# Performance work log

Measured on AMD Instinct MI355X. Metric: run time of the kernel, lower is better.

## Reference

```python
import jax, jax.numpy as jnp
import numpy as np

S = 7          # grid size
B = 2          # boxes per cell
C = 20         # classes
STEP = 1.0 / S
L_COORD = 5.0
L_NOOBJ = 0.5
EPS = 1e-6


def setup_inputs() -> dict:
    key = jax.random.key(0)
    k1, k2, k3 = jax.random.split(key, 3)
    N = 16384
    pred = jax.random.normal(k1, (N, S, S, B * 5 + C), dtype=jnp.float32)
    target = jax.random.uniform(k2, (N, S, S, B * 5 + C), dtype=jnp.float32)
    objm = jax.random.uniform(k3, (N, S, S, B)) < 0.05
    tb = target[..., :10].reshape(N, S, S, B, 5)
    tb = tb.at[..., 4].set(tb[..., 4] * objm)
    target = target.at[..., :10].set(tb.reshape(N, S, S, 10))
    return {"pred": pred, "target": target}


def _convert_box(box, gx, gy):
    # box: [N,S,S,B,4] in cell-relative (x,y) + image-relative (w,h)
    # gx: grid x index (axis 2), gy: grid y index (axis 1); matches conver_box
    x = (box[..., 0] + gx) * STEP - box[..., 2] * 0.5
    y = (box[..., 1] + gy) * STEP - box[..., 3] * 0.5
    out = jnp.stack([x, y, box[..., 2], box[..., 3]], axis=-1)
    return jnp.clip(out, 0.0, 1.0)


def _iou(b1, b2):
    x1, y1, w1, h1 = b1[..., 0], b1[..., 1], b1[..., 2], b1[..., 3]
    x2, y2, w2, h2 = b2[..., 0], b2[..., 1], b2[..., 2], b2[..., 3]
    inter_w = jnp.maximum(w1 + w2 - (jnp.maximum(x1 + w1, x2 + w2) - jnp.minimum(x1, x2)), 0.0)
    inter_h = jnp.maximum(h1 + h2 - (jnp.maximum(y1 + h1, y2 + h2) - jnp.minimum(y1, y2)), 0.0)
    inter = inter_w * inter_h
    union = w1 * h1 + w2 * h2 - inter + EPS
    return inter / union


def reference(pred, target):
    N = pred.shape[0]
    pb = pred[..., :10].reshape(N, S, S, B, 5)   # [N,S,S,B,5]
    tb = target[..., :10].reshape(N, S, S, B, 5)
    pc = pred[..., 10:]                           # [N,S,S,C]
    tc = target[..., 10:]
    obj0 = tb[..., 4] > 0                         # [N,S,S,B]
    sig = jnp.any(obj0, axis=-1)                  # [N,S,S]
    # grid indices: torch loop uses (y=dim1, x=dim2), conver_box index=[x, y]
    gx = jnp.arange(S, dtype=pred.dtype).reshape(1, 1, S, 1)
    gy = jnp.arange(S, dtype=pred.dtype).reshape(1, S, 1, 1)
    ious = _iou(_convert_box(pb[..., :4], gx, gy), _convert_box(tb[..., :4], gx, gy))  # [N,S,S,B]
    # responsible box = argmax IoU (first index on ties, matching torch .max(0))
    best = jnp.argmax(ious, axis=-1)[..., None] == jnp.arange(B)  # [N,S,S,B]
    obj = obj0 & best
    zero = jnp.zeros((), pred.dtype)
    # confidence losses
    dconf2 = (pb[..., 4] - tb[..., 4]) ** 2
    obj_loss = jnp.sum(jnp.where(obj, dconf2, zero))
    noobj_loss = jnp.sum(jnp.where(~obj, dconf2, zero))
    # coordinate losses
    obj_e = obj[..., None]
    dxy2 = (pb[..., :2] - tb[..., :2]) ** 2
    xy_loss = jnp.sum(jnp.where(obj_e, dxy2, zero))
    pwh = jnp.maximum(pb[..., 2:4], 0.0)
    dwh2 = (jnp.sqrt(tb[..., 2:4] + EPS) - jnp.sqrt(pwh + EPS)) ** 2
    wh_loss = jnp.sum(jnp.where(obj_e, dwh2, zero))
    # class loss over cells containing any object
    dcls2 = (pc - tc) ** 2
    class_loss = jnp.sum(jnp.where(sig[..., None], dcls2, zero))
    loss = obj_loss + L_NOOBJ * noobj_loss + L_COORD * xy_loss + L_COORD * wh_loss + class_loss
    return loss / N
```

## Files before the change

kernel.cpp:

```cpp
#include <hip/hip_runtime.h>

#define STEPV (1.0f / 7.0f)
#define L_COORD 5.0f
#define L_NOOBJ 0.5f
#define EPSV 1e-6f

#define TILE 128
#define FLOATS_PER_CELL 30
#define TILE_FLOATS (TILE * FLOATS_PER_CELL)
#define TILE_F4 (TILE_FLOATS / 4)

__global__ __launch_bounds__(256) void yolo_loss_kernel(
    const float* __restrict__ pred,
    const float* __restrict__ tgt,
    float* __restrict__ partials)
{
    __shared__ float bufP[TILE_FLOATS];
    __shared__ float bufT[TILE_FLOATS];

    const int tid = threadIdx.x;
    const int base_f4 = blockIdx.x * TILE_F4;

    {
        const float4* srcP = reinterpret_cast<const float4*>(pred) + base_f4;
        const float4* srcT = reinterpret_cast<const float4*>(tgt) + base_f4;
        float4* dstP = reinterpret_cast<float4*>(bufP);
        float4* dstT = reinterpret_cast<float4*>(bufT);
        #pragma unroll
        for (int i = 0; i < (TILE_F4 + 255) / 256; ++i) {
            int li = tid + i * 256;
            if (li < TILE_F4) {
                dstP[li] = srcP[li];
                dstT[li] = srcT[li];
            }
        }
    }
    __syncthreads();

    const int cid  = tid & (TILE - 1);
    const int half = tid >> 7;
    const int cell = blockIdx.x * TILE + cid;

    float loss = 0.0f;

    if (half == 0) {
        const float* p = bufP + cid * FLOATS_PER_CELL;
        const float* t = bufT + cid * FLOATS_PER_CELL;
        float pv[10], tv[10];
        #pragma unroll
        for (int k = 0; k < 5; ++k) {
            float2 a = *reinterpret_cast<const float2*>(p + 2 * k);
            pv[2 * k] = a.x; pv[2 * k + 1] = a.y;
            float2 b = *reinterpret_cast<const float2*>(t + 2 * k);
            tv[2 * k] = b.x; tv[2 * k + 1] = b.y;
        }

        int ij = cell % 49;
        float gy = (float)(ij / 7);
        float gx = (float)(ij % 7);

        float iou[2];
        #pragma unroll
        for (int b = 0; b < 2; ++b) {
            const float* pb = pv + b * 5;
            const float* tb = tv + b * 5;
            float x1 = fminf(fmaxf((pb[0] + gx) * STEPV - pb[2] * 0.5f, 0.f), 1.f);
            float y1 = fminf(fmaxf((pb[1] + gy) * STEPV - pb[3] * 0.5f, 0.f), 1.f);
            float w1 = fminf(fmaxf(pb[2], 0.f), 1.f);
            float h1 = fminf(fmaxf(pb[3], 0.f), 1.f);
            float x2 = fminf(fmaxf((tb[0] + gx) * STEPV - tb[2] * 0.5f, 0.f), 1.f);
            float y2 = fminf(fmaxf((tb[1] + gy) * STEPV - tb[3] * 0.5f, 0.f), 1.f);
            float w2 = fminf(fmaxf(tb[2], 0.f), 1.f);
            float h2 = fminf(fmaxf(tb[3], 0.f), 1.f);
            float iw = fmaxf(w1 + w2 - (fmaxf(x1 + w1, x2 + w2) - fminf(x1, x2)), 0.f);
            float ih = fmaxf(h1 + h2 - (fmaxf(y1 + h1, y2 + h2) - fminf(y1, y2)), 0.f);
            float inter = iw * ih;
            float uni = w1 * h1 + w2 * h2 - inter + EPSV;
            iou[b] = inter / uni;
        }
        int best = (iou[1] > iou[0]) ? 1 : 0;

        float obj_l = 0.f, noobj_l = 0.f, xy_l = 0.f, wh_l = 0.f;
        #pragma unroll
        for (int b = 0; b < 2; ++b) {
            const float* pb = pv + b * 5;
            const float* tb = tv + b * 5;
            bool obj = (tb[4] > 0.f) && (b == best);
            float dc = pb[4] - tb[4];
            dc *= dc;
            if (obj) {
                obj_l += dc;
                float dx = pb[0] - tb[0];
                float dy = pb[1] - tb[1];
                xy_l += dx * dx + dy * dy;
                float sw = sqrtf(tb[2] + EPSV) - sqrtf(fmaxf(pb[2], 0.f) + EPSV);
                float sh = sqrtf(tb[3] + EPSV) - sqrtf(fmaxf(pb[3], 0.f) + EPSV);
                wh_l += sw * sw + sh * sh;
            } else {
                noobj_l += dc;
            }
        }
        loss = obj_l + L_NOOBJ * noobj_l + L_COORD * (xy_l + wh_l);
    } else {
        const float* p = bufP + cid * FLOATS_PER_CELL + 10;
        const float* t = bufT + cid * FLOATS_PER_CELL + 10;
        float t4 = bufT[cid * FLOATS_PER_CELL + 4];
        float t9 = bufT[cid * FLOATS_PER_CELL + 9];
        bool sig = (t4 > 0.f) || (t9 > 0.f);

        float cls = 0.f;
        #pragma unroll
        for (int k = 0; k < 10; ++k) {
            float2 a = *reinterpret_cast<const float2*>(p + 2 * k);
            float2 b = *reinterpret_cast<const float2*>(t + 2 * k);
            float d0 = a.x - b.x;
            float d1 = a.y - b.y;
            cls += d0 * d0 + d1 * d1;
        }
        loss = sig ? cls : 0.0f;
    }

    #pragma unroll
    for (int off = 32; off > 0; off >>= 1)
        loss += __shfl_down(loss, off, 64);

    __shared__ float wsum[4];
    int lane = tid & 63;
    int wid  = tid >> 6;
    if (lane == 0) wsum[wid] = loss;
    __syncthreads();
    if (tid == 0)
        partials[blockIdx.x] = wsum[0] + wsum[1] + wsum[2] + wsum[3];
}

__global__ __launch_bounds__(256) void yolo_finalize(
    const float* __restrict__ partials,
    float* __restrict__ out, int nparts, float invN)
{
    double s = 0.0;
    for (int i = threadIdx.x; i < nparts; i += 256)
        s += (double)partials[i];

    #pragma unroll
    for (int off = 32; off > 0; off >>= 1)
        s += __shfl_down(s, off, 64);

    __shared__ double wsum[4];
    int lane = threadIdx.x & 63;
    int wid  = threadIdx.x >> 6;
    if (lane == 0) wsum[wid] = s;
    __syncthreads();
    if (threadIdx.x == 0)
        out[0] = (float)((wsum[0] + wsum[1] + wsum[2] + wsum[3]) * (double)invN);
}

extern "C" void kernel_launch(void* const* d_in, const int* in_sizes, int n_in,
                              void* d_out, int out_size, void* d_ws, size_t ws_size,
                              hipStream_t stream)
{
    const float* pred = (const float*)d_in[0];
    const float* tgt  = (const float*)d_in[1];
    float* out      = (float*)d_out;
    float* partials = (float*)d_ws;

    int ncells = in_sizes[0] / FLOATS_PER_CELL;
    int N = ncells / 49;
    int blocks = ncells / TILE;

    yolo_loss_kernel<<<blocks, 256, 0, stream>>>(pred, tgt, partials);
    yolo_finalize<<<1, 256, 0, stream>>>(partials, out, blocks, 1.0f / (float)N);
}
```

Before: 40.73 us.

## Load tiles via global_load_lds with 384-thread blocks and split class work

```diff
diff --git a/kernel.cpp b/kernel.cpp
--- a/kernel.cpp
+++ b/kernel.cpp
@@ -7,43 +7,50 @@
 
 #define TILE 128
 #define FLOATS_PER_CELL 30
-#define TILE_FLOATS (TILE * FLOATS_PER_CELL)
-#define TILE_F4 (TILE_FLOATS / 4)
+#define TILE_F4 (TILE * FLOATS_PER_CELL / 4)
 
-__global__ __launch_bounds__(256) void yolo_loss_kernel(
+typedef const __attribute__((address_space(1))) void cg_void;
+typedef __attribute__((address_space(3))) void ls_void;
+
+__global__ __launch_bounds__(384) void yolo_loss_kernel(
     const float* __restrict__ pred,
     const float* __restrict__ tgt,
     float* __restrict__ partials)
 {
-    __shared__ float bufP[TILE_FLOATS];
-    __shared__ float bufT[TILE_FLOATS];
+    __shared__ float4 bufP4[TILE_F4];
+    __shared__ float4 bufT4[TILE_F4];
 
-    const int tid = threadIdx.x;
-    const int base_f4 = blockIdx.x * TILE_F4;
+    const int tid  = threadIdx.x;
+    const int w    = tid >> 6;
+    const int lane = tid & 63;
 
-    {
-        const float4* srcP = reinterpret_cast<const float4*>(pred) + base_f4;
-        const float4* srcT = reinterpret_cast<const float4*>(tgt) + base_f4;
-        float4* dstP = reinterpret_cast<float4*>(bufP);
-        float4* dstT = reinterpret_cast<float4*>(bufT);
+    if (w < 3) {
+        const float4* g = reinterpret_cast<const float4*>(pred)
+                        + (size_t)blockIdx.x * TILE_F4 + w * 320 + lane;
         #pragma unroll
-        for (int i = 0; i < (TILE_F4 + 255) / 256; ++i) {
-            int li = tid + i * 256;
-            if (li < TILE_F4) {
-                dstP[li] = srcP[li];
-                dstT[li] = srcT[li];
-            }
-        }
+        for (int i = 0; i < 5; ++i)
+            __builtin_amdgcn_global_load_lds((cg_void*)(g + i * 64),
+                                             (ls_void*)(bufP4 + w * 320 + i * 64),
+                                             16, 0, 0);
+    } else {
+        const float4* g = reinterpret_cast<const float4*>(tgt)
+                        + (size_t)blockIdx.x * TILE_F4 + (w - 3) * 320 + lane;
+        #pragma unroll
+        for (int i = 0; i < 5; ++i)
+            __builtin_amdgcn_global_load_lds((cg_void*)(g + i * 64),
+                                             (ls_void*)(bufT4 + (w - 3) * 320 + i * 64),
+                                             16, 0, 0);
     }
     __syncthreads();
 
-    const int cid  = tid & (TILE - 1);
-    const int half = tid >> 7;
-    const int cell = blockIdx.x * TILE + cid;
+    const float* bufP = reinterpret_cast<const float*>(bufP4);
+    const float* bufT = reinterpret_cast<const float*>(bufT4);
 
     float loss = 0.0f;
 
-    if (half == 0) {
+    if (tid < TILE) {
+        const int cid  = tid;
+        const int cell = blockIdx.x * TILE + cid;
         const float* p = bufP + cid * FLOATS_PER_CELL;
         const float* t = bufT + cid * FLOATS_PER_CELL;
         float pv[10], tv[10];
@@ -102,15 +109,18 @@
         }
         loss = obj_l + L_NOOBJ * noobj_l + L_COORD * (xy_l + wh_l);
     } else {
-        const float* p = bufP + cid * FLOATS_PER_CELL + 10;
-        const float* t = bufT + cid * FLOATS_PER_CELL + 10;
+        const int q   = tid - TILE;
+        const int cid = q >> 1;
+        const int sub = q & 1;
+        const float* p = bufP + cid * FLOATS_PER_CELL + 10 + sub * 10;
+        const float* t = bufT + cid * FLOATS_PER_CELL + 10 + sub * 10;
         float t4 = bufT[cid * FLOATS_PER_CELL + 4];
         float t9 = bufT[cid * FLOATS_PER_CELL + 9];
         bool sig = (t4 > 0.f) || (t9 > 0.f);
 
         float cls = 0.f;
         #pragma unroll
-        for (int k = 0; k < 10; ++k) {
+        for (int k = 0; k < 5; ++k) {
             float2 a = *reinterpret_cast<const float2*>(p + 2 * k);
             float2 b = *reinterpret_cast<const float2*>(t + 2 * k);
             float d0 = a.x - b.x;
@@ -124,34 +134,40 @@
     for (int off = 32; off > 0; off >>= 1)
         loss += __shfl_down(loss, off, 64);
 
-    __shared__ float wsum[4];
-    int lane = tid & 63;
-    int wid  = tid >> 6;
-    if (lane == 0) wsum[wid] = loss;
+    __shared__ float wsum[6];
+    if (lane == 0) wsum[w] = loss;
     __syncthreads();
-    if (tid == 0)
-        partials[blockIdx.x] = wsum[0] + wsum[1] + wsum[2] + wsum[3];
+    if (tid == 0) {
+        float s = 0.f;
+        #pragma unroll
+        for (int k = 0; k < 6; ++k) s += wsum[k];
+        partials[blockIdx.x] = s;
+    }
 }
 
-__global__ __launch_bounds__(256) void yolo_finalize(
+__global__ __launch_bounds__(1024) void yolo_finalize(
     const float* __restrict__ partials,
     float* __restrict__ out, int nparts, float invN)
 {
     double s = 0.0;
-    for (int i = threadIdx.x; i < nparts; i += 256)
+    for (int i = threadIdx.x; i < nparts; i += 1024)
         s += (double)partials[i];
 
     #pragma unroll
     for (int off = 32; off > 0; off >>= 1)
         s += __shfl_down(s, off, 64);
 
-    __shared__ double wsum[4];
+    __shared__ double wsum[16];
     int lane = threadIdx.x & 63;
     int wid  = threadIdx.x >> 6;
     if (lane == 0) wsum[wid] = s;
     __syncthreads();
-    if (threadIdx.x == 0)
-        out[0] = (float)((wsum[0] + wsum[1] + wsum[2] + wsum[3]) * (double)invN);
+    if (threadIdx.x == 0) {
+        double tot = 0.0;
+        #pragma unroll
+        for (int k = 0; k < 16; ++k) tot += wsum[k];
+        out[0] = (float)(tot * (double)invN);
+    }
 }
 
 extern "C" void kernel_launch(void* const* d_in, const int* in_sizes, int n_in,
@@ -167,6 +183,6 @@
     int N = ncells / 49;
     int blocks = ncells / TILE;
 
-    yolo_loss_kernel<<<blocks, 256, 0, stream>>>(pred, tgt, partials);
-    yolo_finalize<<<1, 256, 0, stream>>>(partials, out, blocks, 1.0f / (float)N);
+    yolo_loss_kernel<<<blocks, 384, 0, stream>>>(pred, tgt, partials);
+    yolo_finalize<<<1, 1024, 0, stream>>>(partials, out, blocks, 1.0f / (float)N);
 }
```

Measured after the change: 36.22 us, median of 2. -11.1%, faster.
